# Kernel tuning notes

Hardware: AMD Instinct MI355X
Metric: run time of the kernel (lower is better)

## Reference

```python
import jax, jax.numpy as jnp
import numpy as np

B, N = 2, 4096
BN_EPS = 1e-5
INV_STD = np.float32(1.0 / np.sqrt(1.0 + BN_EPS))  # BN inference: running_mean=0, running_var=1


def pconv(x, w):
    # 1x1 Conv1d == per-point matmul: x [B,C,N], w [Cout,Cin] -> [B,Cout,N]
    return jnp.einsum('oc,bcn->bon', w, x)


def bn(x, g, b):
    # inference BatchNorm1d with mean=0, var=1
    return x * (INV_STD * g)[None, :, None] + b[None, :, None]


def sa_layer(x, qk_w, v_w, v_b, t_w, t_b, g, b):
    # PCT offset-attention. q_conv and k_conv share weights, so energy is a Gram matrix.
    xq = pconv(x, qk_w)                                   # [B, C//2, N]
    energy = jnp.einsum('bcn,bcm->bnm', xq, xq)           # [B, N, N]
    att = jax.nn.softmax(energy, axis=-1)
    att = att / (1e-9 + att.sum(axis=1, keepdims=True))   # extra L1 renorm over dim=1
    xv = pconv(x, v_w) + v_b[None, :, None]               # [B, C, N]
    x_r = jnp.einsum('bcn,bnm->bcm', xv, att)             # [B, C, N]
    # offset=True branch
    x_r = jax.nn.relu(bn(pconv(x - x_r, t_w) + t_b[None, :, None], g, b))
    return x + x_r


def _forward(x, conv1_w, bn1_g, bn1_b, conv2_w, bn2_g, bn2_b, conv3_w, bn3_g, bn3_b,
             pt1_w, pt1_g, pt1_b, pt2_w, pt2_g, pt2_b,
             sa1_qk, sa1_vw, sa1_vb, sa1_tw, sa1_tb, sa1_g, sa1_b,
             sa2_qk, sa2_vw, sa2_vb, sa2_tw, sa2_tb, sa2_g, sa2_b,
             cf_w, cf_g, cf_b, s1_w, s1_g, s1_b, s2_w, s2_g, s2_b, s3_w):
    h = jnp.transpose(x, (0, 2, 1))                       # [B, 3, N]
    h = jax.nn.relu(bn(pconv(h, conv1_w), bn1_g, bn1_b))  # [B, 64, N]
    h = jax.nn.relu(bn(pconv(h, conv2_w), bn2_g, bn2_b))  # [B, 128, N]
    h = jax.nn.relu(bn(pconv(h, conv3_w), bn3_g, bn3_b))  # [B, 256, N]
    # Point_Transformer_Last
    h = jax.nn.relu(bn(pconv(h, pt1_w), pt1_g, pt1_b))
    h = jax.nn.relu(bn(pconv(h, pt2_w), pt2_g, pt2_b))
    x1 = sa_layer(h, sa1_qk, sa1_vw, sa1_vb, sa1_tw, sa1_tb, sa1_g, sa1_b)
    x2 = sa_layer(x1, sa2_qk, sa2_vw, sa2_vb, sa2_tw, sa2_tb, sa2_g, sa2_b)
    # original forward reuses sa2's weights for layers 3 and 4
    x3 = sa_layer(x2, sa2_qk, sa2_vw, sa2_vb, sa2_tw, sa2_tb, sa2_g, sa2_b)
    x4 = sa_layer(x3, sa2_qk, sa2_vw, sa2_vb, sa2_tw, sa2_tb, sa2_g, sa2_b)
    h = jnp.concatenate([x1, x2, x3, x4], axis=1)         # [B, 1024, N]
    face = jax.nn.leaky_relu(bn(pconv(h, cf_w), cf_g, cf_b), 0.2)  # [B, 512, N]
    gmax = jnp.max(face, axis=2, keepdims=True)           # adaptive_max_pool1d(.,1)
    h = jnp.concatenate([face, jnp.broadcast_to(gmax, face.shape)], axis=1)  # [B, 1024, N]
    h = jax.nn.leaky_relu(bn(pconv(h, s1_w), s1_g, s1_b), 0.2)
    h = jax.nn.leaky_relu(bn(pconv(h, s2_w), s2_g, s2_b), 0.2)
    h = pconv(h, s3_w)                                    # [B, 50, N]
    return jnp.transpose(h, (0, 2, 1))                    # [B, N, 50]


def setup_inputs() -> dict:
    key = jax.random.key(0)
    kit = iter(jax.random.split(key, 80))
    def W(co, ci):
        return jax.random.normal(next(kit), (co, ci), dtype=jnp.float32) / np.float32(np.sqrt(ci))
    def G(c):
        return 1.0 + 0.1 * jax.random.normal(next(kit), (c,), dtype=jnp.float32)
    def Bv(c):
        return 0.1 * jax.random.normal(next(kit), (c,), dtype=jnp.float32)
    d = {}
    d['x'] = jax.random.normal(next(kit), (B, N, 3), dtype=jnp.float32)
    d['conv1_w'] = W(64, 3);   d['bn1_g'] = G(64);  d['bn1_b'] = Bv(64)
    d['conv2_w'] = W(128, 64); d['bn2_g'] = G(128); d['bn2_b'] = Bv(128)
    d['conv3_w'] = W(256, 128); d['bn3_g'] = G(256); d['bn3_b'] = Bv(256)
    d['pt1_w'] = W(256, 256); d['pt1_g'] = G(256); d['pt1_b'] = Bv(256)
    d['pt2_w'] = W(256, 256); d['pt2_g'] = G(256); d['pt2_b'] = Bv(256)
    for p in ('sa1', 'sa2'):
        d[p + '_qk'] = 0.1 * W(128, 256)  # small scale keeps softmax unsaturated
        d[p + '_vw'] = W(256, 256); d[p + '_vb'] = Bv(256)
        d[p + '_tw'] = W(256, 256); d[p + '_tb'] = Bv(256)
        d[p + '_g'] = G(256); d[p + '_b'] = Bv(256)
    d['cf_w'] = W(512, 1024); d['cf_g'] = G(512); d['cf_b'] = Bv(512)
    d['s1_w'] = W(512, 1024); d['s1_g'] = G(512); d['s1_b'] = Bv(512)
    d['s2_w'] = W(256, 512); d['s2_g'] = G(256); d['s2_b'] = Bv(256)
    d['s3_w'] = W(50, 256)
    return d


def reference(x, conv1_w, bn1_g, bn1_b, conv2_w, bn2_g, bn2_b, conv3_w, bn3_g, bn3_b,
              pt1_w, pt1_g, pt1_b, pt2_w, pt2_g, pt2_b,
              sa1_qk, sa1_vw, sa1_vb, sa1_tw, sa1_tb, sa1_g, sa1_b,
              sa2_qk, sa2_vw, sa2_vb, sa2_tw, sa2_tb, sa2_g, sa2_b,
              cf_w, cf_g, cf_b, s1_w, s1_g, s1_b, s2_w, s2_g, s2_b, s3_w):
    return _forward(x, conv1_w, bn1_g, bn1_b, conv2_w, bn2_g, bn2_b, conv3_w, bn3_g, bn3_b,
                    pt1_w, pt1_g, pt1_b, pt2_w, pt2_g, pt2_b,
                    sa1_qk, sa1_vw, sa1_vb, sa1_tw, sa1_tb, sa1_g, sa1_b,
                    sa2_qk, sa2_vw, sa2_vb, sa2_tw, sa2_tb, sa2_g, sa2_b,
                    cf_w, cf_g, cf_b, s1_w, s1_g, s1_b, s2_w, s2_g, s2_b, s3_w)
```

## Files before the change

### kernel.cpp

```cpp
#include <hip/hip_runtime.h>
#include <hip/hip_bf16.h>


#define NPTS 4096
#define BATCH 2
#define MSPLIT 4
#define RSSPLIT 8
static constexpr float INV_STD = 0.9999950000374997f;

__device__ __forceinline__ float bf2f(unsigned short u) {
    return __uint_as_float(((unsigned int)u) << 16);
}
__device__ __forceinline__ unsigned short f2bf(float f) {
    unsigned int x = __float_as_uint(f);
    unsigned int r = (x + 0x7FFFu + ((x >> 16) & 1u)) >> 16;
    return (unsigned short)r;
}

__device__ __forceinline__ void async16(const unsigned short* g, unsigned short* l)
{
    __builtin_amdgcn_global_load_lds(
        (const __attribute__((address_space(1))) unsigned int*)(const void*)g,
        (__attribute__((address_space(3))) unsigned int*)(void*)l,
        16, 0, 0);
}

typedef __attribute__((ext_vector_type(8))) short short8;
typedef __attribute__((ext_vector_type(4))) float f32x4;

struct WSplit {
    const float* src[14];
    int n[14];
    long long off[14];
};

__global__ __launch_bounds__(256)
void presplit_k(WSplit d, unsigned short* __restrict__ wbuf)
{
    int wi = blockIdx.y;
    int i = blockIdx.x * 256 + threadIdx.x;
    int n = d.n[wi];
    if (i >= n) return;
    float v = d.src[wi][i];
    unsigned short h = f2bf(v);
    unsigned short* dst = wbuf + d.off[wi];
    dst[i] = h;
    dst[n + i] = f2bf(v - bf2f(h));
}

__global__ __launch_bounds__(256)
void gemm_nt_split(const unsigned short* __restrict__ A, long long a_bs, int a_lda, long long a_po,
                   const unsigned short* __restrict__ B, long long b_bs, int b_lda, long long b_po,
                   void* __restrict__ Cp, long long c_bs, int c_ld, long long c_po,
                   int Nb, int K,
                   const float* __restrict__ bias, int bias_mode,
                   const float* __restrict__ bng, const float* __restrict__ bnb,
                   const unsigned short* __restrict__ res, long long res_bs, int res_ld, long long res_po,
                   int act, int out_mode)
{
    __shared__ unsigned short As[2][64 * 64];
    __shared__ unsigned short Bs[2][64 * 64];
    const int b = blockIdx.z;
    const int m0 = blockIdx.y * 64, n0 = blockIdx.x * 64;
    const int t = threadIdx.x;
    const int lane = t & 63, w = t >> 6;
    const int wr = (w >> 1) * 32, wc = (w & 1) * 32;
    const int ml = lane & 15, q = lane >> 4;

    f32x4 acc[2][2] = {};

    for (int k0 = 0; k0 < K; k0 += 64) {
        __syncthreads();
        #pragma unroll
        for (int e = 0; e < 2; e++) {
            int idx = t + e * 256;
            int row = idx >> 3, blk = idx & 7;
            int gblk = blk ^ (row & 7);
            int lofs = (e * 256 + (t & 192)) * 8;
            const unsigned short* sA = A + (long long)b * a_bs
                                     + (long long)(m0 + row) * a_lda + k0 + gblk * 8;
            const unsigned short* sB = B + (long long)b * b_bs
                                     + (long long)(n0 + row) * b_lda + k0 + gblk * 8;
            async16(sA,        &As[0][0] + lofs);
            async16(sA + a_po, &As[1][0] + lofs);
            async16(sB,        &Bs[0][0] + lofs);
            async16(sB + b_po, &Bs[1][0] + lofs);
        }
        __syncthreads();
        #pragma unroll
        for (int kk = 0; kk < 2; kk++) {
            short8 ah[2], al[2], bh[2], bl[2];
            #pragma unroll
            for (int it = 0; it < 2; it++) {
                int row = wr + it * 16 + ml;
                int slot = (kk * 4 + q) ^ (row & 7);
                ah[it] = *(const short8*)(&As[0][row * 64 + slot * 8]);
                al[it] = *(const short8*)(&As[1][row * 64 + slot * 8]);
            }
            #pragma unroll
            for (int jt = 0; jt < 2; jt++) {
                int row = wc + jt * 16 + ml;
                int slot = (kk * 4 + q) ^ (row & 7);
                bh[jt] = *(const short8*)(&Bs[0][row * 64 + slot * 8]);
                bl[jt] = *(const short8*)(&Bs[1][row * 64 + slot * 8]);
            }
            #pragma unroll
            for (int it = 0; it < 2; it++)
                #pragma unroll
                for (int jt = 0; jt < 2; jt++) {
                    acc[it][jt] = __builtin_amdgcn_mfma_f32_16x16x32_bf16(ah[it], bh[jt], acc[it][jt], 0, 0, 0);
                    acc[it][jt] = __builtin_amdgcn_mfma_f32_16x16x32_bf16(ah[it], bl[jt], acc[it][jt], 0, 0, 0);
                    acc[it][jt] = __builtin_amdgcn_mfma_f32_16x16x32_bf16(al[it], bh[jt], acc[it][jt], 0, 0, 0);
                }
        }
    }

    #pragma unroll
    for (int it = 0; it < 2; it++)
        #pragma unroll
        for (int jt = 0; jt < 2; jt++)
            #pragma unroll
            for (int r = 0; r < 4; r++) {
                int rg = m0 + wr + it * 16 + q * 4 + r;
                int cg = n0 + wc + jt * 16 + ml;
                float y = acc[it][jt][r];
                if (bias) {
                    if (bias_mode == 3)      y += bias[rg];
                    else if (bias_mode == 2) y += bias[b * Nb + cg];
                    else                     y += bias[cg];
                }
                if (bng) y = y * (INV_STD * bng[cg]) + bnb[cg];
                if (act == 1) y = fmaxf(y, 0.f);
                else if (act == 2) y = (y > 0.f) ? y : 0.2f * y;
                if (res) {
                    long long ri_ = (long long)b * res_bs + (long long)rg * res_ld + cg;
                    y += bf2f(res[ri_]) + bf2f(res[res_po + ri_]);
                }
                long long ci = (long long)b * c_bs + (long long)rg * c_ld + cg;
                if (out_mode == 0) {
                    unsigned short* C = (unsigned short*)Cp;
                    unsigned short h = f2bf(y);
                    C[ci] = h;
                    C[c_po + ci] = f2bf(y - bf2f(h));
                } else if (out_mode == 1) {
                    ((unsigned short*)Cp)[ci] = f2bf(y);
                } else {
                    if (cg < Nb) ((float*)Cp)[ci] = y;
                }
            }
}

__global__ __launch_bounds__(256)
void rs_k(const unsigned short* __restrict__ xq, float* __restrict__ rs)
{
    __shared__ unsigned short Kq[2][64 * 64];
    const int b = blockIdx.z;
    const int p0 = blockIdx.y * 64;
    const int m_beg = blockIdx.x * (NPTS / RSSPLIT);
    const unsigned short* xqB = xq + (long long)b * NPTS * 128;
    const int t = threadIdx.x;
    const int lane = t & 63, w = t >> 6;
    const int pw = w * 16;
    const int ml = lane & 15, q = lane >> 4;

    short8 af[4];
    #pragma unroll
    for (int ks = 0; ks < 4; ks++)
        af[ks] = *(const short8*)(xqB + (long long)(p0 + pw + ml) * 128 + ks * 32 + q * 8);

    float rsum[4] = {0.f, 0.f, 0.f, 0.f};

    for (int m0 = m_beg; m0 < m_beg + NPTS / RSSPLIT; m0 += 64) {
        __syncthreads();
        #pragma unroll
        for (int e = 0; e < 4; e++) {
            int idx = t + e * 256;
            int sub = idx >> 9, row = (idx >> 3) & 63, blk = idx & 7;
            int gblk = blk ^ (row & 7);
            int lofs = (e * 256 + (t & 192)) * 8;
            async16(xqB + (long long)(m0 + row) * 128 + sub * 64 + gblk * 8,
                    &Kq[0][0] + lofs);
        }
        __syncthreads();
        f32x4 acc[4] = {};
        #pragma unroll
        for (int ks = 0; ks < 4; ks++) {
            int kh = ks >> 1, kk = ks & 1;
            #pragma unroll
            for (int jt = 0; jt < 4; jt++) {
                int row = jt * 16 + ml;
                int slot = (kk * 4 + q) ^ (row & 7);
                short8 bf = *(const short8*)(&Kq[kh][row * 64 + slot * 8]);
                acc[jt] = __builtin_amdgcn_mfma_f32_16x16x32_bf16(af[ks], bf, acc[jt], 0, 0, 0);
            }
        }
        #pragma unroll
        for (int jt = 0; jt < 4; jt++)
            #pragma unroll
            for (int r = 0; r < 4; r++)
                rsum[r] += __expf(acc[jt][r]);
    }
    #pragma unroll
    for (int r = 0; r < 4; r++) {
        float s = rsum[r];
        s += __shfl_xor(s, 1); s += __shfl_xor(s, 2);
        s += __shfl_xor(s, 4); s += __shfl_xor(s, 8);
        if (ml == 0) atomicAdd(&rs[b * NPTS + p0 + pw + q * 4 + r], s);
    }
}

__global__ __launch_bounds__(256)
void attn_pv(const unsigned short* __restrict__ xq,
             const unsigned short* __restrict__ xv,
             const float* __restrict__ rinv,
             float* __restrict__ part,
             float* __restrict__ cs)
{
    __shared__ unsigned short Kq[2][64 * 64];
    __shared__ unsigned short Vv[128 * 64];
    __shared__ unsigned short Pl[64][72];
    const int z = blockIdx.z, b = z / MSPLIT, ms = z % MSPLIT;
    const int c0 = blockIdx.x * 128;
    const int p0 = blockIdx.y * 64;
    const unsigned short* xqB = xq + (long long)b * NPTS * 128;
    const unsigned short* xvB = xv + (long long)b * 256 * NPTS;
    const float* riB = rinv + b * NPTS;
    const int t = threadIdx.x;
    const int lane = t & 63, w = t >> 6;
    const int pw = w * 16;
    const int cw = w * 32;
    const int ml = lane & 15, q = lane >> 4;
    const bool do_cs = (blockIdx.x == 0);

    short8 af[4];
    #pragma unroll
    for (int ks = 0; ks < 4; ks++)
        af[ks] = *(const short8*)(xqB + (long long)(p0 + pw + ml) * 128 + ks * 32 + q * 8);

    f32x4 pv[4][2] = {};
    float csr[4] = {0.f, 0.f, 0.f, 0.f};

    const int m_beg = ms * (NPTS / MSPLIT);
    for (int m0 = m_beg; m0 < m_beg + NPTS / MSPLIT; m0 += 64) {
        __syncthreads();
        #pragma unroll
        for (int e = 0; e < 4; e++) {
            int idx = t + e * 256;
            int sub = idx >> 9, row = (idx >> 3) & 63, blk = idx & 7;
            int gblk = blk ^ (row & 7);
            int lofs = (e * 256 + (t & 192)) * 8;
            async16(xqB + (long long)(m0 + row) * 128 + sub * 64 + gblk * 8,
                    &Kq[0][0] + lofs);
        }
        #pragma unroll
        for (int e = 0; e < 4; e++) {
            int idx = t + e * 256;
            int row = idx >> 3, blk = idx & 7;
            int gblk = blk ^ (row & 7);
            int lofs = (e * 256 + (t & 192)) * 8;
            async16(xvB + (long long)(c0 + row) * NPTS + m0 + gblk * 8, Vv + lofs);
        }
        __syncthreads();
        f32x4 acc[4] = {};
        #pragma unroll
        for (int ks = 0; ks < 4; ks++) {
            int kh = ks >> 1, kk = ks & 1;
            #pragma unroll
            for (int jt = 0; jt < 4; jt++) {
                int row = jt * 16 + ml;
                int slot = (kk * 4 + q) ^ (row & 7);
                short8 bf = *(const short8*)(&Kq[kh][row * 64 + slot * 8]);
                acc[jt] = __builtin_amdgcn_mfma_f32_16x16x32_bf16(af[ks], bf, acc[jt], 0, 0, 0);
            }
        }
        #pragma unroll
        for (int jt = 0; jt < 4; jt++) {
            float rvm = riB[m0 + jt * 16 + ml];
            #pragma unroll
            for (int r = 0; r < 4; r++) {
                float pvv = __expf(acc[jt][r]) * rvm;
                csr[r] += pvv;
                Pl[pw + q * 4 + r][jt * 16 + ml] = f2bf(pvv);
            }
        }
        __syncthreads();
        #pragma unroll
        for (int kk = 0; kk < 2; kk++) {
            short8 ap[4];
            #pragma unroll
            for (int pst = 0; pst < 4; pst++)
                ap[pst] = *(const short8*)(&Pl[pst * 16 + ml][kk * 32 + q * 8]);
            #pragma unroll
            for (int jt = 0; jt < 2; jt++) {
                int row = cw + jt * 16 + ml;
                int slot = (kk * 4 + q) ^ (row & 7);
                short8 bv = *(const short8*)(&Vv[row * 64 + slot * 8]);
                #pragma unroll
                for (int pst = 0; pst < 4; pst++)
                    pv[pst][jt] = __builtin_amdgcn_mfma_f32_16x16x32_bf16(
                        ap[pst], bv, pv[pst][jt], 0, 0, 0);
            }
        }
    }
    if (do_cs) {
        #pragma unroll
        for (int r = 0; r < 4; r++) {
            float s = csr[r];
            s += __shfl_xor(s, 1); s += __shfl_xor(s, 2);
            s += __shfl_xor(s, 4); s += __shfl_xor(s, 8);
            if (ml == 0) atomicAdd(&cs[b * NPTS + p0 + pw + q * 4 + r], s);
        }
    }
    float* C = part + (long long)z * ((long long)NPTS * 256);
    #pragma unroll
    for (int pst = 0; pst < 4; pst++)
        #pragma unroll
        for (int jt = 0; jt < 2; jt++)
            #pragma unroll
            for (int r = 0; r < 4; r++) {
                int rg = p0 + pst * 16 + q * 4 + r;
                int cg = c0 + cw + jt * 16 + ml;
                C[(long long)rg * 256 + cg] = pv[pst][jt][r];
            }
}

__global__ __launch_bounds__(256)
void conv1_k(const float* __restrict__ x, const float* __restrict__ w,
             const float* __restrict__ g, const float* __restrict__ bb,
             unsigned short* __restrict__ h, long long h_po)
{
    int b = blockIdx.y;
    int p = blockIdx.x * 4 + (threadIdx.x >> 6);
    int c = threadIdx.x & 63;
    const float* xp = x + ((long long)b * NPTS + p) * 3;
    float y = xp[0] * w[c * 3] + xp[1] * w[c * 3 + 1] + xp[2] * w[c * 3 + 2];
    y = y * (INV_STD * g[c]) + bb[c];
    y = fmaxf(y, 0.f);
    long long i = ((long long)b * NPTS + p) * 64 + c;
    unsigned short hi = f2bf(y);
    h[i] = hi;
    h[h_po + i] = f2bf(y - bf2f(hi));
}

__global__ __launch_bounds__(256)
void zero_k(float* __restrict__ p, int n)
{
    int i = blockIdx.x * 256 + threadIdx.x;
    if (i < n) p[i] = 0.f;
}

__global__ __launch_bounds__(256)
void recip_k(const float* __restrict__ rs, float* __restrict__ ri, int n)
{
    int i = blockIdx.x * 256 + threadIdx.x;
    if (i < n) ri[i] = 1.f / rs[i];
}

__global__ __launch_bounds__(256)
void diff_k(const unsigned short* __restrict__ xin, long long x_bs, int x_ld, long long x_po,
            const float* __restrict__ part, const float* __restrict__ cs,
            unsigned short* __restrict__ d, long long d_po)
{
    long long i = (long long)blockIdx.x * 256 + threadIdx.x;
    int b = blockIdx.y;
    int p = (int)(i >> 8), c = (int)(i & 255);
    long long xi = (long long)b * x_bs + (long long)p * x_ld + c;
    float xv = bf2f(xin[xi]) + bf2f(xin[x_po + xi]);
    float xr = 0.f;
    #pragma unroll
    for (int ks = 0; ks < MSPLIT; ks++)
        xr += part[((long long)(b * MSPLIT + ks)) * ((long long)NPTS * 256) + i];
    float denom = 1e-9f + cs[b * NPTS + p];
    float v = xv - xr / denom;
    long long di = (long long)b * NPTS * 256 + i;
    unsigned short hi = f2bf(v);
    d[di] = hi;
    d[d_po + di] = f2bf(v - bf2f(hi));
}

__global__ __launch_bounds__(256)
void gmaxp_k(const unsigned short* __restrict__ face, long long f_po, float* __restrict__ pm)
{
    int c = blockIdx.x * 256 + threadIdx.x;
    int ch = blockIdx.y;
    int b = blockIdx.z;
    float m = -3.4e38f;
    for (int j = 0; j < 256; j++) {
        long long i = ((long long)b * NPTS + ch * 256 + j) * 512 + c;
        m = fmaxf(m, bf2f(face[i]) + bf2f(face[f_po + i]));
    }
    pm[((long long)b * 16 + ch) * 512 + c] = m;
}

__global__ __launch_bounds__(256)
void gmaxr_k(const float* __restrict__ pm, float* __restrict__ gm)
{
    int idx = blockIdx.x * 256 + threadIdx.x;
    int b = idx >> 9, c = idx & 511;
    float m = -3.4e38f;
    for (int ch = 0; ch < 16; ch++)
        m = fmaxf(m, pm[((long long)b * 16 + ch) * 512 + c]);
    gm[idx] = m;
}

__global__ __launch_bounds__(256)
void bias2_k(const float* __restrict__ w, const float* __restrict__ g, float* __restrict__ b2)
{
    int o = blockIdx.x * 256 + threadIdx.x;
    int b = blockIdx.y;
    if (o >= 512) return;
    float s = 0.f;
    for (int c = 0; c < 512; c++) s += w[(long long)o * 1024 + 512 + c] * g[b * 512 + c];
    b2[b * 512 + o] = s;
}

extern "C" void kernel_launch(void* const* d_in, const int* in_sizes, int n_in,
                              void* d_out, int out_size, void* d_ws, size_t ws_size,
                              hipStream_t stream)
{
    const float* x       = (const float*)d_in[0];
    const float* conv1_w = (const float*)d_in[1];
    const float* bn1_g   = (const float*)d_in[2];
    const float* bn1_b   = (const float*)d_in[3];
    const float* conv2_w = (const float*)d_in[4];
    const float* bn2_g   = (const float*)d_in[5];
    const float* bn2_b   = (const float*)d_in[6];
    const float* conv3_w = (const float*)d_in[7];
    const float* bn3_g   = (const float*)d_in[8];
    const float* bn3_b   = (const float*)d_in[9];
    const float* pt1_w   = (const float*)d_in[10];
    const float* pt1_g   = (const float*)d_in[11];
    const float* pt1_b   = (const float*)d_in[12];
    const float* pt2_w   = (const float*)d_in[13];
    const float* pt2_g   = (const float*)d_in[14];
    const float* pt2_b   = (const float*)d_in[15];
    const float* sa_qk[2] = {(const float*)d_in[16], (const float*)d_in[23]};
    const float* sa_vw[2] = {(const float*)d_in[17], (const float*)d_in[24]};
    const float* sa_vb[2] = {(const float*)d_in[18], (const float*)d_in[25]};
    const float* sa_tw[2] = {(const float*)d_in[19], (const float*)d_in[26]};
    const float* sa_tb[2] = {(const float*)d_in[20], (const float*)d_in[27]};
    const float* sa_g[2]  = {(const float*)d_in[21], (const float*)d_in[28]};
    const float* sa_b[2]  = {(const float*)d_in[22], (const float*)d_in[29]};
    const float* cf_w = (const float*)d_in[30];
    const float* cf_g = (const float*)d_in[31];
    const float* cf_b = (const float*)d_in[32];
    const float* s1_w = (const float*)d_in[33];
    const float* s1_g = (const float*)d_in[34];
    const float* s1_b = (const float*)d_in[35];
    const float* s2_w = (const float*)d_in[36];
    const float* s2_g = (const float*)d_in[37];
    const float* s2_b = (const float*)d_in[38];
    const float* s3_w = (const float*)d_in[39];

    char* base = (char*)d_ws;
    size_t off = 0;
    auto alloc = [&](size_t bytes) -> void* {
        void* p = base + off;
        off = (off + bytes + 255) & ~(size_t)255;
        return p;
    };
    const long long N = NPTS;
    const long long PO64   = (long long)BATCH * N * 64;
    const long long PO128  = (long long)BATCH * N * 128;
    const long long PO256  = (long long)BATCH * N * 256;
    const long long PO512  = (long long)BATCH * N * 512;
    const long long PO1024 = (long long)BATCH * N * 1024;

    unsigned short* S1  = (unsigned short*)alloc(2 * PO256 * 2);
    unsigned short* S2  = (unsigned short*)alloc(2 * PO256 * 2);
    unsigned short* Dv  = (unsigned short*)alloc(2 * PO256 * 2);
    unsigned short* cat = (unsigned short*)alloc(2 * PO1024 * 2);
    unsigned short* face = (unsigned short*)alloc(2 * PO512 * 2);
    unsigned short* xq  = (unsigned short*)alloc((size_t)BATCH * N * 128 * 2);
    unsigned short* xv  = (unsigned short*)alloc((size_t)BATCH * 256 * N * 2);
    unsigned short* s1b = (unsigned short*)alloc(2 * PO512 * 2);
    unsigned short* s2b = (unsigned short*)alloc(2 * PO256 * 2);
    float* part = (float*)alloc((size_t)BATCH * MSPLIT * N * 256 * 4);
    float* rs = (float*)alloc((size_t)BATCH * N * 4);
    float* cs = (float*)alloc((size_t)BATCH * N * 4);
    float* ri = (float*)alloc((size_t)BATCH * N * 4);
    float* pm = (float*)alloc((size_t)BATCH * 16 * 512 * 4);
    float* gm = (float*)alloc((size_t)BATCH * 512 * 4);
    float* b2 = (float*)alloc((size_t)BATCH * 512 * 4);
    unsigned short* wb = (unsigned short*)alloc((size_t)3400000 * 2);

    WSplit wd;
    const float* wsrc[14] = {conv2_w, conv3_w, pt1_w, pt2_w, sa_qk[0], sa_qk[1],
                             sa_vw[0], sa_vw[1], sa_tw[0], sa_tw[1], cf_w, s1_w, s2_w, s3_w};
    int wn[14] = {128*64, 256*128, 256*256, 256*256, 128*256, 128*256,
                  256*256, 256*256, 256*256, 256*256, 512*1024, 512*1024, 256*512, 50*256};
    long long wo[14]; long long acc_ = 0;
    for (int i = 0; i < 14; i++) { wd.src[i] = wsrc[i]; wd.n[i] = wn[i]; wd.off[i] = acc_; wo[i] = acc_; acc_ += 2LL * wn[i]; }
    presplit_k<<<dim3((512*1024 + 255) / 256, 14), 256, 0, stream>>>(wd, wb);
    auto W = [&](int i) { return wb + wo[i]; };

    auto nt = [&](const unsigned short* A, long long a_bs, int a_lda, long long a_po,
                  const unsigned short* B, long long b_bs, int b_lda, long long b_po,
                  void* C, long long c_bs, int c_ld, long long c_po,
                  int Mrows, int Nb, int K,
                  const float* bias, int bias_mode,
                  const float* bng, const float* bnb,
                  const unsigned short* res, long long res_bs, int res_ld, long long res_po,
                  int act, int out_mode) {
        dim3 g((Nb + 63) / 64, Mrows / 64, BATCH);
        gemm_nt_split<<<g, 256, 0, stream>>>(A, a_bs, a_lda, a_po, B, b_bs, b_lda, b_po,
                                             C, c_bs, c_ld, c_po, Nb, K,
                                             bias, bias_mode, bng, bnb,
                                             res, res_bs, res_ld, res_po, act, out_mode);
    };

    conv1_k<<<dim3(NPTS / 4, BATCH), 256, 0, stream>>>(x, conv1_w, bn1_g, bn1_b, S1, PO64);
    nt(S1, N * 64, 64, PO64,    W(0), 0, 64, wn[0],  S2, N * 128, 128, PO128,
       NPTS, 128, 64,  nullptr, 0, bn2_g, bn2_b, nullptr, 0, 0, 0, 1, 0);
    nt(S2, N * 128, 128, PO128, W(1), 0, 128, wn[1], S1, N * 256, 256, PO256,
       NPTS, 256, 128, nullptr, 0, bn3_g, bn3_b, nullptr, 0, 0, 0, 1, 0);
    nt(S1, N * 256, 256, PO256, W(2), 0, 256, wn[2], S2, N * 256, 256, PO256,
       NPTS, 256, 256, nullptr, 0, pt1_g, pt1_b, nullptr, 0, 0, 0, 1, 0);
    nt(S2, N * 256, 256, PO256, W(3), 0, 256, wn[3], S1, N * 256, 256, PO256,
       NPTS, 256, 256, nullptr, 0, pt2_g, pt2_b, nullptr, 0, 0, 0, 1, 0);

    for (int i = 0; i < 4; i++) {
        int p = (i == 0) ? 0 : 1;
        const unsigned short* xin = (i == 0) ? S1 : cat + (size_t)(i - 1) * 256;
        long long xin_bs = (i == 0) ? N * 256 : N * 1024;
        int xin_ld = (i == 0) ? 256 : 1024;
        long long xin_po = (i == 0) ? PO256 : PO1024;

        nt(xin, xin_bs, xin_ld, xin_po, W(4 + p), 0, 256, wn[4 + p],
           xq, N * 128, 128, 0, NPTS, 128, 256,
           nullptr, 0, nullptr, nullptr, nullptr, 0, 0, 0, 0, 1);
        nt(W(6 + p), 0, 256, wn[6 + p], xin, xin_bs, xin_ld, xin_po,
           xv, 256 * N, NPTS, 0, 256, NPTS, 256,
           sa_vb[p], 3, nullptr, nullptr, nullptr, 0, 0, 0, 0, 1);
        zero_k<<<(2 * BATCH * NPTS + 255) / 256, 256, 0, stream>>>(rs, 2 * BATCH * NPTS);
        rs_k<<<dim3(RSSPLIT, NPTS / 64, BATCH), 256, 0, stream>>>(xq, rs);
        recip_k<<<(BATCH * NPTS + 255) / 256, 256, 0, stream>>>(rs, ri, BATCH * NPTS);
        attn_pv<<<dim3(2, NPTS / 64, BATCH * MSPLIT), 256, 0, stream>>>(
            xq, xv, ri, part, cs);
        diff_k<<<dim3(NPTS * 256 / 256, BATCH), 256, 0, stream>>>(
            xin, xin_bs, xin_ld, xin_po, part, cs, Dv, PO256);
        nt(Dv, N * 256, 256, PO256, W(8 + p), 0, 256, wn[8 + p],
           cat + (size_t)i * 256, N * 1024, 1024, PO1024,
           NPTS, 256, 256, sa_tb[p], 1, sa_g[p], sa_b[p],
           xin, xin_bs, xin_ld, xin_po, 1, 0);
    }

    nt(cat, N * 1024, 1024, PO1024, W(10), 0, 1024, wn[10],
       face, N * 512, 512, PO512, NPTS, 512, 1024,
       nullptr, 0, cf_g, cf_b, nullptr, 0, 0, 0, 2, 0);
    gmaxp_k<<<dim3(2, 16, BATCH), 256, 0, stream>>>(face, PO512, pm);
    gmaxr_k<<<dim3(BATCH * 512 / 256), 256, 0, stream>>>(pm, gm);
    bias2_k<<<dim3(2, BATCH), 256, 0, stream>>>(s1_w, gm, b2);
    nt(face, N * 512, 512, PO512, W(11), 0, 1024, wn[11],
       s1b, N * 512, 512, PO512, NPTS, 512, 512,
       b2, 2, s1_g, s1_b, nullptr, 0, 0, 0, 2, 0);
    nt(s1b, N * 512, 512, PO512, W(12), 0, 512, wn[12],
       s2b, N * 256, 256, PO256, NPTS, 256, 512,
       nullptr, 0, s2_g, s2_b, nullptr, 0, 0, 0, 2, 0);
    nt(s2b, N * 256, 256, PO256, W(13), 0, 256, wn[13],
       d_out, N * 50, 50, 0, NPTS, 50, 256,
       nullptr, 0, nullptr, nullptr, nullptr, 0, 0, 0, 0, 2);
}
```

Measured before the change: 906.6 us.

## Cover all 256 value channels per attention block to avoid recomputing QK^T exp

attn_pv now processes all 256 output channels in a single block instead of splitting channels across two blocks. Each 64-row attention tile's Gram product and exponentials are therefore computed once rather than twice. Column sums are written as per-split partials and summed in diff_k instead of being accumulated with atomics, and the separate reciprocal kernel is folded into attn_pv as an inline division. In exchange the grid is half as large, the block's LDS for V doubles to 32KB, and the accumulator register count doubles, which may reduce occupancy.

```diff
diff --git a/kernel.cpp b/kernel.cpp
--- a/kernel.cpp
+++ b/kernel.cpp
@@ -212,32 +212,30 @@
 __global__ __launch_bounds__(256)
 void attn_pv(const unsigned short* __restrict__ xq,
              const unsigned short* __restrict__ xv,
-             const float* __restrict__ rinv,
+             const float* __restrict__ rs,
              float* __restrict__ part,
-             float* __restrict__ cs)
+             float* __restrict__ csp)
 {
     __shared__ unsigned short Kq[2][64 * 64];
-    __shared__ unsigned short Vv[128 * 64];
+    __shared__ unsigned short Vv[256 * 64];
     __shared__ unsigned short Pl[64][72];
     const int z = blockIdx.z, b = z / MSPLIT, ms = z % MSPLIT;
-    const int c0 = blockIdx.x * 128;
     const int p0 = blockIdx.y * 64;
     const unsigned short* xqB = xq + (long long)b * NPTS * 128;
     const unsigned short* xvB = xv + (long long)b * 256 * NPTS;
-    const float* riB = rinv + b * NPTS;
+    const float* rsB = rs + b * NPTS;
     const int t = threadIdx.x;
     const int lane = t & 63, w = t >> 6;
     const int pw = w * 16;
-    const int cw = w * 32;
+    const int cw = w * 64;
     const int ml = lane & 15, q = lane >> 4;
-    const bool do_cs = (blockIdx.x == 0);
 
     short8 af[4];
     #pragma unroll
     for (int ks = 0; ks < 4; ks++)
         af[ks] = *(const short8*)(xqB + (long long)(p0 + pw + ml) * 128 + ks * 32 + q * 8);
 
-    f32x4 pv[4][2] = {};
+    f32x4 pv[4][4] = {};
     float csr[4] = {0.f, 0.f, 0.f, 0.f};
 
     const int m_beg = ms * (NPTS / MSPLIT);
@@ -253,12 +251,12 @@
                     &Kq[0][0] + lofs);
         }
         #pragma unroll
-        for (int e = 0; e < 4; e++) {
+        for (int e = 0; e < 8; e++) {
             int idx = t + e * 256;
             int row = idx >> 3, blk = idx & 7;
             int gblk = blk ^ (row & 7);
             int lofs = (e * 256 + (t & 192)) * 8;
-            async16(xvB + (long long)(c0 + row) * NPTS + m0 + gblk * 8, Vv + lofs);
+            async16(xvB + (long long)row * NPTS + m0 + gblk * 8, Vv + lofs);
         }
         __syncthreads();
         f32x4 acc[4] = {};
@@ -275,7 +273,7 @@
         }
         #pragma unroll
         for (int jt = 0; jt < 4; jt++) {
-            float rvm = riB[m0 + jt * 16 + ml];
+            float rvm = 1.f / rsB[m0 + jt * 16 + ml];
             #pragma unroll
             for (int r = 0; r < 4; r++) {
                 float pvv = __expf(acc[jt][r]) * rvm;
@@ -291,7 +289,7 @@
             for (int pst = 0; pst < 4; pst++)
                 ap[pst] = *(const short8*)(&Pl[pst * 16 + ml][kk * 32 + q * 8]);
             #pragma unroll
-            for (int jt = 0; jt < 2; jt++) {
+            for (int jt = 0; jt < 4; jt++) {
                 int row = cw + jt * 16 + ml;
                 int slot = (kk * 4 + q) ^ (row & 7);
                 short8 bv = *(const short8*)(&Vv[row * 64 + slot * 8]);
@@ -302,24 +300,22 @@
             }
         }
     }
-    if (do_cs) {
-        #pragma unroll
-        for (int r = 0; r < 4; r++) {
-            float s = csr[r];
-            s += __shfl_xor(s, 1); s += __shfl_xor(s, 2);
-            s += __shfl_xor(s, 4); s += __shfl_xor(s, 8);
-            if (ml == 0) atomicAdd(&cs[b * NPTS + p0 + pw + q * 4 + r], s);
-        }
+    #pragma unroll
+    for (int r = 0; r < 4; r++) {
+        float s = csr[r];
+        s += __shfl_xor(s, 1); s += __shfl_xor(s, 2);
+        s += __shfl_xor(s, 4); s += __shfl_xor(s, 8);
+        if (ml == 0) csp[(long long)z * NPTS + p0 + pw + q * 4 + r] = s;
     }
     float* C = part + (long long)z * ((long long)NPTS * 256);
     #pragma unroll
     for (int pst = 0; pst < 4; pst++)
         #pragma unroll
-        for (int jt = 0; jt < 2; jt++)
+        for (int jt = 0; jt < 4; jt++)
             #pragma unroll
             for (int r = 0; r < 4; r++) {
                 int rg = p0 + pst * 16 + q * 4 + r;
-                int cg = c0 + cw + jt * 16 + ml;
+                int cg = cw + jt * 16 + ml;
                 C[(long long)rg * 256 + cg] = pv[pst][jt][r];
             }
 }
@@ -350,15 +346,8 @@
 }
 
 __global__ __launch_bounds__(256)
-void recip_k(const float* __restrict__ rs, float* __restrict__ ri, int n)
-{
-    int i = blockIdx.x * 256 + threadIdx.x;
-    if (i < n) ri[i] = 1.f / rs[i];
-}
-
-__global__ __launch_bounds__(256)
 void diff_k(const unsigned short* __restrict__ xin, long long x_bs, int x_ld, long long x_po,
-            const float* __restrict__ part, const float* __restrict__ cs,
+            const float* __restrict__ part, const float* __restrict__ csp,
             unsigned short* __restrict__ d, long long d_po)
 {
     long long i = (long long)blockIdx.x * 256 + threadIdx.x;
@@ -366,12 +355,14 @@
     int p = (int)(i >> 8), c = (int)(i & 255);
     long long xi = (long long)b * x_bs + (long long)p * x_ld + c;
     float xv = bf2f(xin[xi]) + bf2f(xin[x_po + xi]);
-    float xr = 0.f;
-    #pragma unroll
-    for (int ks = 0; ks < MSPLIT; ks++)
-        xr += part[((long long)(b * MSPLIT + ks)) * ((long long)NPTS * 256) + i];
-    float denom = 1e-9f + cs[b * NPTS + p];
-    float v = xv - xr / denom;
+    float xr = 0.f, den = 1e-9f;
+    #pragma unroll
+    for (int ks = 0; ks < MSPLIT; ks++) {
+        int z = b * MSPLIT + ks;
+        xr  += part[(long long)z * ((long long)NPTS * 256) + i];
+        den += csp[(long long)z * NPTS + p];
+    }
+    float v = xv - xr / den;
     long long di = (long long)b * NPTS * 256 + i;
     unsigned short hi = f2bf(v);
     d[di] = hi;
@@ -476,9 +467,8 @@
     unsigned short* s1b = (unsigned short*)alloc(2 * PO512 * 2);
     unsigned short* s2b = (unsigned short*)alloc(2 * PO256 * 2);
     float* part = (float*)alloc((size_t)BATCH * MSPLIT * N * 256 * 4);
+    float* csp  = (float*)alloc((size_t)BATCH * MSPLIT * N * 4);
     float* rs = (float*)alloc((size_t)BATCH * N * 4);
-    float* cs = (float*)alloc((size_t)BATCH * N * 4);
-    float* ri = (float*)alloc((size_t)BATCH * N * 4);
     float* pm = (float*)alloc((size_t)BATCH * 16 * 512 * 4);
     float* gm = (float*)alloc((size_t)BATCH * 512 * 4);
     float* b2 = (float*)alloc((size_t)BATCH * 512 * 4);
@@ -532,13 +522,12 @@
         nt(W(6 + p), 0, 256, wn[6 + p], xin, xin_bs, xin_ld, xin_po,
            xv, 256 * N, NPTS, 0, 256, NPTS, 256,
            sa_vb[p], 3, nullptr, nullptr, nullptr, 0, 0, 0, 0, 1);
-        zero_k<<<(2 * BATCH * NPTS + 255) / 256, 256, 0, stream>>>(rs, 2 * BATCH * NPTS);
+        zero_k<<<(BATCH * NPTS + 255) / 256, 256, 0, stream>>>(rs, BATCH * NPTS);
         rs_k<<<dim3(RSSPLIT, NPTS / 64, BATCH), 256, 0, stream>>>(xq, rs);
-        recip_k<<<(BATCH * NPTS + 255) / 256, 256, 0, stream>>>(rs, ri, BATCH * NPTS);
-        attn_pv<<<dim3(2, NPTS / 64, BATCH * MSPLIT), 256, 0, stream>>>(
-            xq, xv, ri, part, cs);
+        attn_pv<<<dim3(1, NPTS / 64, BATCH * MSPLIT), 256, 0, stream>>>(
+            xq, xv, rs, part, csp);
         diff_k<<<dim3(NPTS * 256 / 256, BATCH), 256, 0, stream>>>(
-            xin, xin_bs, xin_ld, xin_po, part, cs, Dv, PO256);
+            xin, xin_bs, xin_ld, xin_po, part, csp, Dv, PO256);
         nt(Dv, N * 256, 256, PO256, W(8 + p), 0, 256, wn[8 + p],
            cat + (size_t)i * 256, N * 1024, 1024, PO1024,
            NPTS, 256, 256, sa_tb[p], 1, sa_g[p], sa_b[p],
```

After: 794.8 us. 1.14x faster.
